# Optimization experiments

Measured on AMD Instinct MI355X. Metric: run time of the kernel, lower is better.

Reference implementation:

```python
import jax, jax.numpy as jnp
import numpy as np

HIDDEN = 4096
N_HEADS = 32
N_KV_HEADS = 8
HEAD_DIM = 128
ROPE_THETA = 1e6
RMS_EPS = 1e-6
SEQ = 2048


def setup_inputs() -> dict:
    key = jax.random.key(0)
    k1, k2, k3 = jax.random.split(key, 3)
    hidden_states = jax.random.normal(k1, (SEQ, HIDDEN), dtype=jnp.float32)
    # fused QKV weight: [hidden, (H + 2*Hkv) * head_dim]
    qkv_out = (N_HEADS + 2 * N_KV_HEADS) * HEAD_DIM
    w_qkv = jax.random.normal(k2, (HIDDEN, qkv_out), dtype=jnp.float32) * (HIDDEN ** -0.5)
    w_o = jax.random.normal(k3, (N_HEADS * HEAD_DIM, HIDDEN), dtype=jnp.float32) * ((N_HEADS * HEAD_DIM) ** -0.5)
    q_norm_w = jnp.ones((HEAD_DIM,), dtype=jnp.float32)
    k_norm_w = jnp.ones((HEAD_DIM,), dtype=jnp.float32)
    # NeoX-style rotary tables [T, head_dim/2]
    pos = jnp.arange(SEQ, dtype=jnp.float32)
    inv_freq = 1.0 / (ROPE_THETA ** (jnp.arange(0, HEAD_DIM, 2, dtype=jnp.float32) / HEAD_DIM))
    freqs = pos[:, None] * inv_freq[None, :]  # [T, d/2]
    cos = jnp.cos(freqs)
    sin = jnp.sin(freqs)
    return {"hidden_states": hidden_states, "cos": cos, "sin": sin,
            "w_qkv": w_qkv, "w_o": w_o, "q_norm_w": q_norm_w, "k_norm_w": k_norm_w}


def _rms_norm(x, w, eps=RMS_EPS):
    # per-head RMSNorm over last dim (head_dim)
    var = jnp.mean(jnp.square(x), axis=-1, keepdims=True)
    return x * jax.lax.rsqrt(var + eps) * w


def _rope(x, cos, sin):
    # NeoX rotate-half: x split into two halves of head_dim
    d2 = x.shape[-1] // 2
    x1, x2 = x[..., :d2], x[..., d2:]
    c = cos[:, None, :]  # [T,1,d/2] broadcast over heads
    s = sin[:, None, :]
    return jnp.concatenate([x1 * c - x2 * s, x2 * c + x1 * s], axis=-1)


def reference(hidden_states, cos, sin, w_qkv, w_o, q_norm_w, k_norm_w):
    T = hidden_states.shape[0]
    H, Hkv, D = N_HEADS, N_KV_HEADS, HEAD_DIM
    G = H // Hkv  # GQA group size
    scale = D ** -0.5

    qkv = hidden_states @ w_qkv  # [T, (H+2Hkv)*D]
    q, k, v = jnp.split(qkv, [H * D, (H + Hkv) * D], axis=1)
    q = q.reshape(T, H, D)
    k = k.reshape(T, Hkv, D)
    v = v.reshape(T, Hkv, D)

    q = _rms_norm(q, q_norm_w)
    k = _rms_norm(k, k_norm_w)
    q = _rope(q, cos, sin)
    k = _rope(k, cos, sin)

    # GQA: group query heads onto shared KV heads
    qg = q.reshape(T, Hkv, G, D)
    scores = jnp.einsum('qhgd,khd->hgqk', qg, k) * scale  # [Hkv,G,T,T]
    causal = jnp.tril(jnp.ones((T, T), dtype=bool))
    scores = jnp.where(causal, scores, jnp.float32(-1e30))
    probs = jax.nn.softmax(scores, axis=-1)
    out = jnp.einsum('hgqk,khd->qhgd', probs, v).reshape(T, H * D)
    return out @ w_o  # [T, hidden]
```

## Files before the change

kernel.cpp:

```cpp
#include <hip/hip_runtime.h>
#include <stdint.h>

#define SEQ   2048
#define HID   4096
#define NQH   32
#define NKVH  8
#define HD    128
#define QKVN  6144

typedef uint16_t u16;
typedef __attribute__((ext_vector_type(8))) short bf16x8;
typedef __attribute__((ext_vector_type(4))) float f32x4;
typedef __attribute__((ext_vector_type(4))) unsigned int u32x4;

static __device__ __forceinline__ float bf2f(u16 h){
  union { float f; unsigned int u; } v; v.u = ((unsigned int)h) << 16; return v.f;
}
static __device__ __forceinline__ u16 f2bf(float f){
  unsigned int u = __float_as_uint(f);
  return (u16)((u + 0x7fffu + ((u >> 16) & 1u)) >> 16);
}
static __device__ __forceinline__ f32x4 mfma16(bf16x8 a, bf16x8 b, f32x4 c){
  return __builtin_amdgcn_mfma_f32_16x16x32_bf16(a, b, c, 0, 0, 0);
}
static __device__ __forceinline__ void gload16(const void* g, void* l){
  __builtin_amdgcn_global_load_lds((const __attribute__((address_space(1))) void*)g,
                                   (__attribute__((address_space(3))) void*)l, 16, 0, 0);
}

__global__ void k_cvt(const float* __restrict__ src, u16* __restrict__ dst, int n4){
  int i = blockIdx.x * blockDim.x + threadIdx.x;
  if (i >= n4) return;
  float4 v = ((const float4*)src)[i];
  uint2 o;
  o.x = (unsigned)f2bf(v.x) | ((unsigned)f2bf(v.y) << 16);
  o.y = (unsigned)f2bf(v.z) | ((unsigned)f2bf(v.w) << 16);
  ((uint2*)dst)[i] = o;
}

__global__ void k_transpose_cvt(const float* __restrict__ src, u16* __restrict__ dst, int K, int N){
  __shared__ float t[32][33];
  int n0 = blockIdx.x * 32, k0 = blockIdx.y * 32;
  int tx = threadIdx.x, ty = threadIdx.y;
#pragma unroll
  for (int i = 0; i < 32; i += 8)
    t[ty + i][tx] = src[(size_t)(k0 + ty + i) * N + n0 + tx];
  __syncthreads();
#pragma unroll
  for (int i = 0; i < 32; i += 8)
    dst[(size_t)(n0 + ty + i) * K + k0 + tx] = f2bf(t[tx][ty + i]);
}

template<int OUTBF>
__global__ __launch_bounds__(256) void k_gemm(const u16* __restrict__ A, const u16* __restrict__ Bt,
                                              void* __restrict__ Cv, int M, int N, int K){
  __shared__ __align__(16) u16 Asm[128][32];
  __shared__ __align__(16) u16 Bsm[128][32];
  int tid = threadIdx.x, lane = tid & 63, wid = tid >> 6;
  int wr = wid >> 1, wc = wid & 1;
  int l16 = lane & 15, lhi = lane >> 4;
  size_t brow = (size_t)blockIdx.y * 128, bcol = (size_t)blockIdx.x * 128;
  const f32x4 vz = {0.f, 0.f, 0.f, 0.f};
  f32x4 acc[4][4];
#pragma unroll
  for (int m = 0; m < 4; m++)
#pragma unroll
    for (int n = 0; n < 4; n++) acc[m][n] = vz;
  int srow = wid * 32 + (lane >> 2);
  int scol = (lane & 3) * 8;
  const u16* Ag = A + (brow + srow) * (size_t)K + scol;
  const u16* Bg = Bt + (bcol + srow) * (size_t)K + scol;
  u16* Al0 = &Asm[wid * 32][0];
  u16* Al1 = &Asm[wid * 32 + 16][0];
  u16* Bl0 = &Bsm[wid * 32][0];
  u16* Bl1 = &Bsm[wid * 32 + 16][0];
  for (int kt = 0; kt < K; kt += 32){
    __syncthreads();
    gload16(Ag + kt, Al0);
    gload16(Ag + (size_t)16 * K + kt, Al1);
    gload16(Bg + kt, Bl0);
    gload16(Bg + (size_t)16 * K + kt, Bl1);
    __syncthreads();
    bf16x8 af[4], bfr[4];
#pragma unroll
    for (int m = 0; m < 4; m++) af[m]  = *(const bf16x8*)&Asm[wr*64 + m*16 + l16][lhi*8];
#pragma unroll
    for (int n = 0; n < 4; n++) bfr[n] = *(const bf16x8*)&Bsm[wc*64 + n*16 + l16][lhi*8];
#pragma unroll
    for (int m = 0; m < 4; m++)
#pragma unroll
      for (int n = 0; n < 4; n++) acc[m][n] = mfma16(af[m], bfr[n], acc[m][n]);
  }
  int rbase = wr*64 + lhi*4, cbase = wc*64 + l16;
#pragma unroll
  for (int m = 0; m < 4; m++)
#pragma unroll
    for (int n = 0; n < 4; n++)
#pragma unroll
      for (int i = 0; i < 4; i++){
        size_t row = brow + rbase + m*16 + i;
        size_t col = bcol + cbase + n*16;
        if (OUTBF) ((u16*)Cv)[row * (size_t)N + col] = f2bf(acc[m][n][i]);
        else       ((float*)Cv)[row * (size_t)N + col] = acc[m][n][i];
      }
}

__global__ __launch_bounds__(256) void k_rmsrope(const u16* __restrict__ qkv, const float* __restrict__ cosp,
                                                 const float* __restrict__ sinp, const float* __restrict__ qw,
                                                 const float* __restrict__ kw, u16* __restrict__ Qr,
                                                 u16* __restrict__ Kr){
  int t = blockIdx.x;
  int lane = threadIdx.x & 63, w = threadIdx.x >> 6;
  int hh = blockIdx.y * 4 + w;
  bool isq = hh < NQH;
  int hl = isq ? hh : hh - NQH;
  const u16* src = qkv + (size_t)t * QKVN + (isq ? hl * HD : NQH * HD + hl * HD);
  unsigned u = *(const unsigned*)(src + 2 * lane);
  float x0 = bf2f((u16)(u & 0xffffu)), x1 = bf2f((u16)(u >> 16));
  float ss = x0 * x0 + x1 * x1;
#pragma unroll
  for (int m = 1; m < 64; m <<= 1) ss += __shfl_xor(ss, m);
  float rs = rsqrtf(ss * (1.f / HD) + 1e-6f);
  const float* wp = isq ? qw : kw;
  float w0 = wp[2 * lane], w1 = wp[2 * lane + 1];
  float xn0 = x0 * rs * w0, xn1 = x1 * rs * w1;
  float p0 = __shfl_xor(xn0, 32), p1 = __shfl_xor(xn1, 32);
  int j0 = (2 * lane) & 63;
  float c0 = cosp[t * 64 + j0], c1 = cosp[t * 64 + j0 + 1];
  float s0 = sinp[t * 64 + j0], s1 = sinp[t * 64 + j0 + 1];
  float o0, o1;
  if (lane < 32){ o0 = xn0 * c0 - p0 * s0; o1 = xn1 * c1 - p1 * s1; }
  else          { o0 = xn0 * c0 + p0 * s0; o1 = xn1 * c1 + p1 * s1; }
  if (isq){ o0 *= 0.08838834764831845f; o1 *= 0.08838834764831845f; }
  u16* dst = isq ? (Qr + ((size_t)hl * SEQ + t) * HD) : (Kr + ((size_t)hl * SEQ + t) * HD);
  *(unsigned*)(dst + 2 * lane) = (unsigned)f2bf(o0) | ((unsigned)f2bf(o1) << 16);
}

__global__ void k_vt(const u16* __restrict__ qkv, u16* __restrict__ VT){
  __shared__ u16 t[32][33];
  int t0 = blockIdx.x * 32, d0 = blockIdx.y * 32, hv = blockIdx.z;
  int tx = threadIdx.x, ty = threadIdx.y;
#pragma unroll
  for (int i = 0; i < 32; i += 8)
    t[ty + i][tx] = qkv[(size_t)(t0 + ty + i) * QKVN + (NQH + NKVH) * HD + hv * HD + d0 + tx];
  __syncthreads();
#pragma unroll
  for (int i = 0; i < 32; i += 8)
    VT[((size_t)hv * HD + d0 + ty + i) * SEQ + t0 + tx] = t[tx][ty + i];
}

__global__ __launch_bounds__(512, 2) void k_attn(const u16* __restrict__ Q, const u16* __restrict__ Kg,
                                                 const u16* __restrict__ VTg, u16* __restrict__ AO){
  __shared__ __align__(16) u16 Ksm[2][64][128];
  __shared__ __align__(16) u16 Vsm[2][128][64];
  __shared__ __align__(16) u16 Psm[8][16][72];
  int tid = threadIdx.x, lane = tid & 63, wid = tid >> 6;
  int l16 = lane & 15, lhi = lane >> 4;
  int bid = blockIdx.x;
  int kvg = bid & 7, rr = bid >> 3;
  int J = 15 - (rr >> 2);
  int hq = kvg * 4 + (rr & 3);
  int qb = J * 128;
  const u16* Kh = Kg  + (size_t)kvg * SEQ * HD;
  const u16* Vh = VTg + (size_t)kvg * HD * SEQ;
  const u16* Qh = Q   + (size_t)hq * SEQ * HD;

  bf16x8 qf[4];
#pragma unroll
  for (int ks = 0; ks < 4; ks++)
    qf[ks] = *(const bf16x8*)(Qh + (size_t)(qb + wid*16 + l16) * HD + ks*32 + lhi*8);

  const f32x4 vz = {0.f, 0.f, 0.f, 0.f};
  f32x4 o[8];
  float mrow[4], lrow[4];
#pragma unroll
  for (int n = 0; n < 8; n++) o[n] = vz;
#pragma unroll
  for (int i = 0; i < 4; i++){ mrow[i] = -1e30f; lrow[i] = 0.f; }

  int krl0 = wid*8 + (lane >> 4), krl1 = krl0 + 4;
  int kgs  = lane & 15;
  const u16* ks0 = Kh + (size_t)krl0 * HD + ((kgs ^ (krl0 & 7)) << 3);
  const u16* ks1 = Kh + (size_t)krl1 * HD + ((kgs ^ (krl1 & 7)) << 3);
  int vrl0 = wid*16 + (lane >> 3), vrl1 = vrl0 + 8;
  int vgs  = lane & 7;
  const u16* vs0 = Vh + (size_t)vrl0 * SEQ + ((vgs ^ (vrl0 & 7)) << 3);
  const u16* vs1 = Vh + (size_t)vrl1 * SEQ + ((vgs ^ (vrl1 & 7)) << 3);

  gload16(ks0, &Ksm[0][wid*8][0]);
  gload16(ks1, &Ksm[0][wid*8 + 4][0]);
  gload16(vs0, &Vsm[0][wid*16][0]);
  gload16(vs1, &Vsm[0][wid*16 + 8][0]);
  __syncthreads();

  int ntr = 2*J + 2;
  int wrow0 = qb + wid*16;
  for (int t = 0; t < ntr; t++){
    int cur = t & 1, nxt = cur ^ 1;
    int kt0 = t << 6;
    if (t < ntr - 1){
      size_t ko = (size_t)(t + 1) * 64 * HD;
      gload16(ks0 + ko, &Ksm[nxt][wid*8][0]);
      gload16(ks1 + ko, &Ksm[nxt][wid*8 + 4][0]);
      int vo = (t + 1) * 64;
      gload16(vs0 + vo, &Vsm[nxt][wid*16][0]);
      gload16(vs1 + vo, &Vsm[nxt][wid*16 + 8][0]);
    }
    if (kt0 <= wrow0 + 15){
      f32x4 s[4];
#pragma unroll
      for (int n = 0; n < 4; n++) s[n] = vz;
      const u16* kbase = &Ksm[cur][0][0];
#pragma unroll
      for (int n = 0; n < 4; n++){
        int row = n*16 + l16, rx = row & 7;
#pragma unroll
        for (int ks = 0; ks < 4; ks++){
          bf16x8 kf = *(const bf16x8*)(kbase + row*128 + (((ks*4 + lhi) ^ rx) << 3));
          s[n] = mfma16(qf[ks], kf, s[n]);
        }
      }
      if (kt0 + 63 > wrow0){
#pragma unroll
        for (int n = 0; n < 4; n++)
#pragma unroll
          for (int i = 0; i < 4; i++)
            if (kt0 + n*16 + l16 > wrow0 + lhi*4 + i) s[n][i] = -1e30f;
      }
#pragma unroll
      for (int i = 0; i < 4; i++){
        float tm = fmaxf(fmaxf(s[0][i], s[1][i]), fmaxf(s[2][i], s[3][i]));
        tm = fmaxf(tm, __shfl_xor(tm, 1));
        tm = fmaxf(tm, __shfl_xor(tm, 2));
        tm = fmaxf(tm, __shfl_xor(tm, 4));
        tm = fmaxf(tm, __shfl_xor(tm, 8));
        float nm = fmaxf(mrow[i], tm);
        float sc = __expf(mrow[i] - nm);
        mrow[i] = nm;
        float rsum = 0.f;
#pragma unroll
        for (int n = 0; n < 4; n++){
          float p = __expf(s[n][i] - nm);
          s[n][i] = p;
          rsum += p;
        }
        rsum += __shfl_xor(rsum, 1);
        rsum += __shfl_xor(rsum, 2);
        rsum += __shfl_xor(rsum, 4);
        rsum += __shfl_xor(rsum, 8);
        lrow[i] = lrow[i] * sc + rsum;
#pragma unroll
        for (int n = 0; n < 8; n++) o[n][i] *= sc;
      }
#pragma unroll
      for (int n = 0; n < 4; n++)
#pragma unroll
        for (int i = 0; i < 4; i++)
          Psm[wid][lhi*4 + i][n*16 + l16] = f2bf(s[n][i]);
      const u16* vbase = &Vsm[cur][0][0];
#pragma unroll
      for (int ksv = 0; ksv < 2; ksv++){
        bf16x8 pa = *(const bf16x8*)&Psm[wid][l16][ksv*32 + lhi*8];
#pragma unroll
        for (int n = 0; n < 8; n++){
          int row = n*16 + l16;
          bf16x8 vb = *(const bf16x8*)(vbase + row*64 + ((((ksv*4) + lhi) ^ (row & 7)) << 3));
          o[n] = mfma16(pa, vb, o[n]);
        }
      }
    }
    if (t < ntr - 1) __syncthreads();
  }
  float inv[4];
#pragma unroll
  for (int i = 0; i < 4; i++) inv[i] = 1.f / lrow[i];
#pragma unroll
  for (int n = 0; n < 8; n++)
#pragma unroll
    for (int i = 0; i < 4; i++){
      int trow = wrow0 + lhi*4 + i;
      AO[(size_t)trow * HID + hq * HD + n*16 + l16] = f2bf(o[n][i] * inv[i]);
    }
}

extern "C" void kernel_launch(void* const* d_in, const int* in_sizes, int n_in,
                              void* d_out, int out_size, void* d_ws, size_t ws_size,
                              hipStream_t stream){
  const float* hs   = (const float*)d_in[0];
  const float* cosp = (const float*)d_in[1];
  const float* sinp = (const float*)d_in[2];
  const float* wqkv = (const float*)d_in[3];
  const float* wo   = (const float*)d_in[4];
  const float* qw   = (const float*)d_in[5];
  const float* kw   = (const float*)d_in[6];
  float* out = (float*)d_out;
  char* ws = (char*)d_ws;
  u16* XB    = (u16*)(ws + 0);
  u16* WQKVT = (u16*)(ws + 16777216);
  u16* WOT   = (u16*)(ws + 0);
  u16* QKV   = (u16*)(ws + 67108864);
  u16* QR    = (u16*)(ws + 92274688);
  u16* KR    = (u16*)(ws + 109051904);
  u16* VTB   = (u16*)(ws + 113246208);
  u16* AOB   = (u16*)(ws + 117440512);

  k_cvt<<<(SEQ * HID / 4 + 255) / 256, 256, 0, stream>>>(hs, XB, SEQ * HID / 4);
  k_transpose_cvt<<<dim3(QKVN / 32, HID / 32), dim3(32, 8), 0, stream>>>(wqkv, WQKVT, HID, QKVN);
  k_gemm<1><<<dim3(QKVN / 128, SEQ / 128), 256, 0, stream>>>(XB, WQKVT, QKV, SEQ, QKVN, HID);
  k_transpose_cvt<<<dim3(HID / 32, HID / 32), dim3(32, 8), 0, stream>>>(wo, WOT, HID, HID);
  k_rmsrope<<<dim3(SEQ, 10), 256, 0, stream>>>(QKV, cosp, sinp, qw, kw, QR, KR);
  k_vt<<<dim3(SEQ / 32, HD / 32, NKVH), dim3(32, 8), 0, stream>>>(QKV, VTB);
  k_attn<<<512, 512, 0, stream>>>(QR, KR, VTB, AOB);
  k_gemm<0><<<dim3(HID / 128, SEQ / 128), 256, 0, stream>>>(AOB, WOT, out, SEQ, HID, HID);
}
```

Measured before the change: 397.6 us.

## Rewrite GEMM with triple-buffered LDS pipeline, 128x256 tiles and swizzled loads

Replaces the GEMM kernel with a 512-thread, 128x256-tile version that triple-buffers K=64 slices in shared memory. Global-to-LDS loads for tile t+2 are interleaved with MFMA phases, coordinated by barriers, explicit waitcnt, sched_barrier and setprio. LDS rows are XOR-swizzled to avoid bank conflicts. The aim is to hide memory latency and remove the serialized load-then-compute pattern of the old single-buffered kernel, at the cost of far more shared memory per block (lower occupancy) and fragile hand-written synchronization.

```diff
diff --git a/kernel.cpp b/kernel.cpp
--- a/kernel.cpp
+++ b/kernel.cpp
@@ -52,56 +52,134 @@
 }
 
 template<int OUTBF>
-__global__ __launch_bounds__(256) void k_gemm(const u16* __restrict__ A, const u16* __restrict__ Bt,
+__global__ __launch_bounds__(512) void k_gemm(const u16* __restrict__ A, const u16* __restrict__ Bt,
                                               void* __restrict__ Cv, int M, int N, int K){
-  __shared__ __align__(16) u16 Asm[128][32];
-  __shared__ __align__(16) u16 Bsm[128][32];
-  int tid = threadIdx.x, lane = tid & 63, wid = tid >> 6;
-  int wr = wid >> 1, wc = wid & 1;
-  int l16 = lane & 15, lhi = lane >> 4;
-  size_t brow = (size_t)blockIdx.y * 128, bcol = (size_t)blockIdx.x * 128;
+  __shared__ __align__(16) u16 Asm[3][128][64];
+  __shared__ __align__(16) u16 Bsm[3][256][64];
+  const int tid = threadIdx.x, lane = tid & 63, wid = tid >> 6;
+  const int wm = wid >> 2, wn = wid & 3;
+  const int l16 = lane & 15, lhi = lane >> 4;
+  const int rx = l16 & 7;
+  const size_t brow = (size_t)blockIdx.y * 128, bcol = (size_t)blockIdx.x * 256;
+
   const f32x4 vz = {0.f, 0.f, 0.f, 0.f};
   f32x4 acc[4][4];
 #pragma unroll
   for (int m = 0; m < 4; m++)
 #pragma unroll
     for (int n = 0; n < 4; n++) acc[m][n] = vz;
-  int srow = wid * 32 + (lane >> 2);
-  int scol = (lane & 3) * 8;
-  const u16* Ag = A + (brow + srow) * (size_t)K + scol;
-  const u16* Bg = Bt + (bcol + srow) * (size_t)K + scol;
-  u16* Al0 = &Asm[wid * 32][0];
-  u16* Al1 = &Asm[wid * 32 + 16][0];
-  u16* Bl0 = &Bsm[wid * 32][0];
-  u16* Bl1 = &Bsm[wid * 32 + 16][0];
-  for (int kt = 0; kt < K; kt += 32){
-    __syncthreads();
-    gload16(Ag + kt, Al0);
-    gload16(Ag + (size_t)16 * K + kt, Al1);
-    gload16(Bg + kt, Bl0);
-    gload16(Bg + (size_t)16 * K + kt, Bl1);
-    __syncthreads();
-    bf16x8 af[4], bfr[4];
-#pragma unroll
-    for (int m = 0; m < 4; m++) af[m]  = *(const bf16x8*)&Asm[wr*64 + m*16 + l16][lhi*8];
-#pragma unroll
-    for (int n = 0; n < 4; n++) bfr[n] = *(const bf16x8*)&Bsm[wc*64 + n*16 + l16][lhi*8];
-#pragma unroll
-    for (int m = 0; m < 4; m++)
-#pragma unroll
-      for (int n = 0; n < 4; n++) acc[m][n] = mfma16(af[m], bfr[n], acc[m][n]);
+
+  const int sg   = (lane & 7) ^ (lane >> 3);
+  const int srow = wid * 8 + (lane >> 3);
+  const u16* Ags = A  + (brow + srow) * (size_t)K + sg * 8;
+  const u16* Bgs = Bt + (bcol + srow) * (size_t)K + sg * 8;
+  const int NT = K >> 6;
+
+#pragma unroll
+  for (int t0 = 0; t0 < 2; t0++){
+    size_t ko = (size_t)t0 * 64;
+    gload16(Ags + ko,                   &Asm[t0][      wid*8][0]);
+    gload16(Ags + (size_t) 64*K + ko,   &Asm[t0][ 64 + wid*8][0]);
+    gload16(Bgs + ko,                   &Bsm[t0][      wid*8][0]);
+    gload16(Bgs + (size_t) 64*K + ko,   &Bsm[t0][ 64 + wid*8][0]);
+    gload16(Bgs + (size_t)128*K + ko,   &Bsm[t0][128 + wid*8][0]);
+    gload16(Bgs + (size_t)192*K + ko,   &Bsm[t0][192 + wid*8][0]);
   }
-  int rbase = wr*64 + lhi*4, cbase = wc*64 + l16;
-#pragma unroll
-  for (int m = 0; m < 4; m++)
-#pragma unroll
-    for (int n = 0; n < 4; n++)
+  asm volatile("s_waitcnt vmcnt(6)" ::: "memory");
+  __builtin_amdgcn_sched_barrier(0);
+  __builtin_amdgcn_s_barrier();
+
+  for (int t = 0; t < NT; ++t){
+    const int c = t % 3, s = (t + 2) % 3;
+    const size_t ko = (size_t)(t + 2) * 64;
+    const bool st = (t + 2 < NT);
+    bf16x8 a0[4], a1[4], b0a, b0b, b1a, b1b;
+#pragma unroll
+    for (int mi = 0; mi < 4; ++mi)
+      a0[mi] = *(const bf16x8*)&Asm[c][wm*64 + mi*16 + l16][(lhi ^ rx) << 3];
+    b0a = *(const bf16x8*)&Bsm[c][wn*64 +  0 + l16][(lhi ^ rx) << 3];
+    b0b = *(const bf16x8*)&Bsm[c][wn*64 + 16 + l16][(lhi ^ rx) << 3];
+    if (st){
+      gload16(Ags + ko,                 &Asm[s][      wid*8][0]);
+      gload16(Ags + (size_t)64*K + ko,  &Asm[s][ 64 + wid*8][0]);
+    }
+    __builtin_amdgcn_s_barrier();
+    asm volatile("s_waitcnt lgkmcnt(0)" ::: "memory");
+    __builtin_amdgcn_sched_barrier(0);
+    __builtin_amdgcn_s_setprio(1);
+#pragma unroll
+    for (int mi = 0; mi < 4; ++mi){
+      acc[mi][0] = mfma16(a0[mi], b0a, acc[mi][0]);
+      acc[mi][1] = mfma16(a0[mi], b0b, acc[mi][1]);
+    }
+    __builtin_amdgcn_s_setprio(0);
+    __builtin_amdgcn_s_barrier();
+    b1a = *(const bf16x8*)&Bsm[c][wn*64 + 32 + l16][(lhi ^ rx) << 3];
+    b1b = *(const bf16x8*)&Bsm[c][wn*64 + 48 + l16][(lhi ^ rx) << 3];
+    if (st) gload16(Bgs + ko, &Bsm[s][wid*8][0]);
+    __builtin_amdgcn_s_barrier();
+    asm volatile("s_waitcnt lgkmcnt(0)" ::: "memory");
+    __builtin_amdgcn_sched_barrier(0);
+    __builtin_amdgcn_s_setprio(1);
+#pragma unroll
+    for (int mi = 0; mi < 4; ++mi){
+      acc[mi][2] = mfma16(a0[mi], b1a, acc[mi][2]);
+      acc[mi][3] = mfma16(a0[mi], b1b, acc[mi][3]);
+    }
+    __builtin_amdgcn_s_setprio(0);
+    __builtin_amdgcn_s_barrier();
+#pragma unroll
+    for (int mi = 0; mi < 4; ++mi)
+      a1[mi] = *(const bf16x8*)&Asm[c][wm*64 + mi*16 + l16][((4 + lhi) ^ rx) << 3];
+    b0a = *(const bf16x8*)&Bsm[c][wn*64 +  0 + l16][((4 + lhi) ^ rx) << 3];
+    b0b = *(const bf16x8*)&Bsm[c][wn*64 + 16 + l16][((4 + lhi) ^ rx) << 3];
+    if (st){
+      gload16(Bgs + (size_t) 64*K + ko, &Bsm[s][ 64 + wid*8][0]);
+      gload16(Bgs + (size_t)128*K + ko, &Bsm[s][128 + wid*8][0]);
+    }
+    __builtin_amdgcn_s_barrier();
+    asm volatile("s_waitcnt lgkmcnt(0)" ::: "memory");
+    __builtin_amdgcn_sched_barrier(0);
+    __builtin_amdgcn_s_setprio(1);
+#pragma unroll
+    for (int mi = 0; mi < 4; ++mi){
+      acc[mi][0] = mfma16(a1[mi], b0a, acc[mi][0]);
+      acc[mi][1] = mfma16(a1[mi], b0b, acc[mi][1]);
+    }
+    __builtin_amdgcn_s_setprio(0);
+    __builtin_amdgcn_s_barrier();
+    b1a = *(const bf16x8*)&Bsm[c][wn*64 + 32 + l16][((4 + lhi) ^ rx) << 3];
+    b1b = *(const bf16x8*)&Bsm[c][wn*64 + 48 + l16][((4 + lhi) ^ rx) << 3];
+    if (st){
+      gload16(Bgs + (size_t)192*K + ko, &Bsm[s][192 + wid*8][0]);
+      asm volatile("s_waitcnt vmcnt(6)" ::: "memory");
+    } else {
+      asm volatile("s_waitcnt vmcnt(0)" ::: "memory");
+    }
+    __builtin_amdgcn_sched_barrier(0);
+    __builtin_amdgcn_s_barrier();
+    asm volatile("s_waitcnt lgkmcnt(0)" ::: "memory");
+    __builtin_amdgcn_sched_barrier(0);
+    __builtin_amdgcn_s_setprio(1);
+#pragma unroll
+    for (int mi = 0; mi < 4; ++mi){
+      acc[mi][2] = mfma16(a1[mi], b1a, acc[mi][2]);
+      acc[mi][3] = mfma16(a1[mi], b1b, acc[mi][3]);
+    }
+    __builtin_amdgcn_s_setprio(0);
+    __builtin_amdgcn_s_barrier();
+  }
+
+#pragma unroll
+  for (int mi = 0; mi < 4; mi++)
+#pragma unroll
+    for (int ni = 0; ni < 4; ni++)
 #pragma unroll
       for (int i = 0; i < 4; i++){
-        size_t row = brow + rbase + m*16 + i;
-        size_t col = bcol + cbase + n*16;
-        if (OUTBF) ((u16*)Cv)[row * (size_t)N + col] = f2bf(acc[m][n][i]);
-        else       ((float*)Cv)[row * (size_t)N + col] = acc[m][n][i];
+        size_t row = brow + wm*64 + mi*16 + lhi*4 + i;
+        size_t col = bcol + wn*64 + ni*16 + l16;
+        if (OUTBF) ((u16*)Cv)[row * (size_t)N + col] = f2bf(acc[mi][ni][i]);
+        else       ((float*)Cv)[row * (size_t)N + col] = acc[mi][ni][i];
       }
 }
 
@@ -213,10 +291,10 @@
       const u16* kbase = &Ksm[cur][0][0];
 #pragma unroll
       for (int n = 0; n < 4; n++){
-        int row = n*16 + l16, rx = row & 7;
+        int row = n*16 + l16, rxk = row & 7;
 #pragma unroll
         for (int ks = 0; ks < 4; ks++){
-          bf16x8 kf = *(const bf16x8*)(kbase + row*128 + (((ks*4 + lhi) ^ rx) << 3));
+          bf16x8 kf = *(const bf16x8*)(kbase + row*128 + (((ks*4 + lhi) ^ rxk) << 3));
           s[n] = mfma16(qf[ks], kf, s[n]);
         }
       }
@@ -306,10 +384,10 @@
 
   k_cvt<<<(SEQ * HID / 4 + 255) / 256, 256, 0, stream>>>(hs, XB, SEQ * HID / 4);
   k_transpose_cvt<<<dim3(QKVN / 32, HID / 32), dim3(32, 8), 0, stream>>>(wqkv, WQKVT, HID, QKVN);
-  k_gemm<1><<<dim3(QKVN / 128, SEQ / 128), 256, 0, stream>>>(XB, WQKVT, QKV, SEQ, QKVN, HID);
+  k_gemm<1><<<dim3(QKVN / 256, SEQ / 128), 512, 0, stream>>>(XB, WQKVT, QKV, SEQ, QKVN, HID);
   k_transpose_cvt<<<dim3(HID / 32, HID / 32), dim3(32, 8), 0, stream>>>(wo, WOT, HID, HID);
   k_rmsrope<<<dim3(SEQ, 10), 256, 0, stream>>>(QKV, cosp, sinp, qw, kw, QR, KR);
   k_vt<<<dim3(SEQ / 32, HD / 32, NKVH), dim3(32, 8), 0, stream>>>(QKV, VTB);
   k_attn<<<512, 512, 0, stream>>>(QR, KR, VTB, AOB);
-  k_gemm<0><<<dim3(HID / 128, SEQ / 128), 256, 0, stream>>>(AOB, WOT, out, SEQ, HID, HID);
-}
+  k_gemm<0><<<dim3(HID / 256, SEQ / 128), 512, 0, stream>>>(AOB, WOT, out, SEQ, HID, HID);
+}
```

New measurement: 459.4 us. 1.16x slower.

## Rewrite GEMM with 4-stage LDS pipeline, 128x256 tiles, swizzle and interleaved MFMA

Applied to the files above, without the earlier changes.

The bf16 GEMM kernel is restructured to use 512 threads and 128x256 output tiles, with a 4-deep ring of LDS buffers filled by direct global-to-LDS loads issued three tiles ahead. Fragment reads for the next tile are interleaved with MFMA groups under explicit waitcnt, sched_barrier and setprio control, and a single s_barrier per k-step replaces the two __syncthreads. An XOR swizzle on the LDS column index is meant to avoid bank conflicts. This aims to hide global and LDS latency in both projections. In exchange it uses more LDS per block, gives fewer blocks for the output GEMM, and depends on fragile hand-tuned wait counts.

```diff
diff --git a/kernel.cpp b/kernel.cpp
--- a/kernel.cpp
+++ b/kernel.cpp
@@ -51,57 +51,114 @@
     dst[(size_t)(n0 + ty + i) * K + k0 + tx] = f2bf(t[tx][ty + i]);
 }
 
+#define FRAG_A(buf, mi) (*(const bf16x8*)&Asm[buf][wm*64 + (mi)*16 + l16][(lhi ^ swz) << 3])
+#define FRAG_B(buf, ni) (*(const bf16x8*)&Bsm[buf][wn*64 + (ni)*16 + l16][(lhi ^ swz) << 3])
+
+#define TILE(T, aC, b01C, b23C, aN, b01N)                                      \
+  do {                                                                         \
+    const int bufc_ = (T) & 3;                                                 \
+    b23C[0] = FRAG_B(bufc_, 2);                                                \
+    b23C[1] = FRAG_B(bufc_, 3);                                                \
+    asm volatile("s_waitcnt lgkmcnt(2)" ::: "memory");                         \
+    __builtin_amdgcn_sched_barrier(0);                                         \
+    __builtin_amdgcn_s_setprio(1);                                             \
+    acc[0][0] = mfma16(aC[0], b01C[0], acc[0][0]);                             \
+    acc[1][0] = mfma16(aC[1], b01C[0], acc[1][0]);                             \
+    acc[2][0] = mfma16(aC[2], b01C[0], acc[2][0]);                             \
+    acc[3][0] = mfma16(aC[3], b01C[0], acc[3][0]);                             \
+    acc[0][1] = mfma16(aC[0], b01C[1], acc[0][1]);                             \
+    acc[1][1] = mfma16(aC[1], b01C[1], acc[1][1]);                             \
+    acc[2][1] = mfma16(aC[2], b01C[1], acc[2][1]);                             \
+    acc[3][1] = mfma16(aC[3], b01C[1], acc[3][1]);                             \
+    __builtin_amdgcn_s_setprio(0);                                             \
+    if ((T) + 1 < NT){                                                         \
+      const int bufn_ = ((T) + 1) & 3;                                         \
+      aN[0] = FRAG_A(bufn_, 0); aN[1] = FRAG_A(bufn_, 1);                      \
+      aN[2] = FRAG_A(bufn_, 2); aN[3] = FRAG_A(bufn_, 3);                      \
+      b01N[0] = FRAG_B(bufn_, 0); b01N[1] = FRAG_B(bufn_, 1);                  \
+      asm volatile("s_waitcnt lgkmcnt(6)" ::: "memory");                       \
+    } else {                                                                   \
+      asm volatile("s_waitcnt lgkmcnt(0)" ::: "memory");                       \
+    }                                                                          \
+    __builtin_amdgcn_sched_barrier(0);                                         \
+    __builtin_amdgcn_s_setprio(1);                                             \
+    acc[0][2] = mfma16(aC[0], b23C[0], acc[0][2]);                             \
+    acc[1][2] = mfma16(aC[1], b23C[0], acc[1][2]);                             \
+    acc[2][2] = mfma16(aC[2], b23C[0], acc[2][2]);                             \
+    acc[3][2] = mfma16(aC[3], b23C[0], acc[3][2]);                             \
+    acc[0][3] = mfma16(aC[0], b23C[1], acc[0][3]);                             \
+    acc[1][3] = mfma16(aC[1], b23C[1], acc[1][3]);                             \
+    acc[2][3] = mfma16(aC[2], b23C[1], acc[2][3]);                             \
+    acc[3][3] = mfma16(aC[3], b23C[1], acc[3][3]);                             \
+    __builtin_amdgcn_s_setprio(0);                                             \
+    if ((T) + 3 < NT){                                                         \
+      const int bufs_ = ((T) + 3) & 3;                                         \
+      const size_t ko_ = (size_t)((T) + 3) * 32;                               \
+      gload16(Ags + ko_, &Asm[bufs_][wid*16][0]);                              \
+      gload16(Bgs + ko_, &Bsm[bufs_][wid*16][0]);                              \
+      gload16(Bgs + (size_t)128*K + ko_, &Bsm[bufs_][128 + wid*16][0]);        \
+      asm volatile("s_waitcnt vmcnt(3)" ::: "memory");                         \
+    } else {                                                                   \
+      asm volatile("s_waitcnt vmcnt(0)" ::: "memory");                         \
+    }                                                                          \
+    __builtin_amdgcn_sched_barrier(0);                                         \
+    __builtin_amdgcn_s_barrier();                                              \
+  } while(0)
+
 template<int OUTBF>
-__global__ __launch_bounds__(256) void k_gemm(const u16* __restrict__ A, const u16* __restrict__ Bt,
+__global__ __launch_bounds__(512) void k_gemm(const u16* __restrict__ A, const u16* __restrict__ Bt,
                                               void* __restrict__ Cv, int M, int N, int K){
-  __shared__ __align__(16) u16 Asm[128][32];
-  __shared__ __align__(16) u16 Bsm[128][32];
-  int tid = threadIdx.x, lane = tid & 63, wid = tid >> 6;
-  int wr = wid >> 1, wc = wid & 1;
-  int l16 = lane & 15, lhi = lane >> 4;
-  size_t brow = (size_t)blockIdx.y * 128, bcol = (size_t)blockIdx.x * 128;
+  __shared__ __align__(16) u16 Asm[4][128][32];
+  __shared__ __align__(16) u16 Bsm[4][256][32];
+  const int tid = threadIdx.x, lane = tid & 63, wid = tid >> 6;
+  const int wm = wid >> 2, wn = wid & 3;
+  const int l16 = lane & 15, lhi = lane >> 4;
+  const int swz = (l16 >> 1) & 3;
+  const size_t brow = (size_t)blockIdx.y * 128, bcol = (size_t)blockIdx.x * 256;
+
   const f32x4 vz = {0.f, 0.f, 0.f, 0.f};
   f32x4 acc[4][4];
 #pragma unroll
   for (int m = 0; m < 4; m++)
 #pragma unroll
     for (int n = 0; n < 4; n++) acc[m][n] = vz;
-  int srow = wid * 32 + (lane >> 2);
-  int scol = (lane & 3) * 8;
-  const u16* Ag = A + (brow + srow) * (size_t)K + scol;
-  const u16* Bg = Bt + (bcol + srow) * (size_t)K + scol;
-  u16* Al0 = &Asm[wid * 32][0];
-  u16* Al1 = &Asm[wid * 32 + 16][0];
-  u16* Bl0 = &Bsm[wid * 32][0];
-  u16* Bl1 = &Bsm[wid * 32 + 16][0];
-  for (int kt = 0; kt < K; kt += 32){
-    __syncthreads();
-    gload16(Ag + kt, Al0);
-    gload16(Ag + (size_t)16 * K + kt, Al1);
-    gload16(Bg + kt, Bl0);
-    gload16(Bg + (size_t)16 * K + kt, Bl1);
-    __syncthreads();
-    bf16x8 af[4], bfr[4];
-#pragma unroll
-    for (int m = 0; m < 4; m++) af[m]  = *(const bf16x8*)&Asm[wr*64 + m*16 + l16][lhi*8];
-#pragma unroll
-    for (int n = 0; n < 4; n++) bfr[n] = *(const bf16x8*)&Bsm[wc*64 + n*16 + l16][lhi*8];
-#pragma unroll
-    for (int m = 0; m < 4; m++)
-#pragma unroll
-      for (int n = 0; n < 4; n++) acc[m][n] = mfma16(af[m], bfr[n], acc[m][n]);
+
+  const int srow = wid * 16 + (lane >> 2);
+  const int sgr  = ((lane & 3) ^ ((lane >> 3) & 3)) * 8;
+  const u16* Ags = A  + (brow + srow) * (size_t)K + sgr;
+  const u16* Bgs = Bt + (bcol + srow) * (size_t)K + sgr;
+  const int NT = K >> 5;
+
+#pragma unroll
+  for (int t0 = 0; t0 < 3; ++t0){
+    const size_t ko = (size_t)t0 * 32;
+    gload16(Ags + ko, &Asm[t0][wid*16][0]);
+    gload16(Bgs + ko, &Bsm[t0][wid*16][0]);
+    gload16(Bgs + (size_t)128*K + ko, &Bsm[t0][128 + wid*16][0]);
   }
-  int rbase = wr*64 + lhi*4, cbase = wc*64 + l16;
-#pragma unroll
-  for (int m = 0; m < 4; m++)
-#pragma unroll
-    for (int n = 0; n < 4; n++)
+  asm volatile("s_waitcnt vmcnt(3)" ::: "memory");
+  __builtin_amdgcn_sched_barrier(0);
+  __builtin_amdgcn_s_barrier();
+
+  bf16x8 aA[4], aB[4], b01A[2], b01B[2], b23A[2], b23B[2];
+  aA[0] = FRAG_A(0, 0); aA[1] = FRAG_A(0, 1); aA[2] = FRAG_A(0, 2); aA[3] = FRAG_A(0, 3);
+  b01A[0] = FRAG_B(0, 0); b01A[1] = FRAG_B(0, 1);
+
+  for (int u = 0; u < (NT >> 1); ++u){
+    TILE(2*u,     aA, b01A, b23A, aB, b01B);
+    TILE(2*u + 1, aB, b01B, b23B, aA, b01A);
+  }
+
+#pragma unroll
+  for (int mi = 0; mi < 4; mi++)
+#pragma unroll
+    for (int ni = 0; ni < 4; ni++)
 #pragma unroll
       for (int i = 0; i < 4; i++){
-        size_t row = brow + rbase + m*16 + i;
-        size_t col = bcol + cbase + n*16;
-        if (OUTBF) ((u16*)Cv)[row * (size_t)N + col] = f2bf(acc[m][n][i]);
-        else       ((float*)Cv)[row * (size_t)N + col] = acc[m][n][i];
+        size_t row = brow + wm*64 + mi*16 + lhi*4 + i;
+        size_t col = bcol + wn*64 + ni*16 + l16;
+        if (OUTBF) ((u16*)Cv)[row * (size_t)N + col] = f2bf(acc[mi][ni][i]);
+        else       ((float*)Cv)[row * (size_t)N + col] = acc[mi][ni][i];
       }
 }
 
@@ -213,10 +270,10 @@
       const u16* kbase = &Ksm[cur][0][0];
 #pragma unroll
       for (int n = 0; n < 4; n++){
-        int row = n*16 + l16, rx = row & 7;
+        int row = n*16 + l16, rxk = row & 7;
 #pragma unroll
         for (int ks = 0; ks < 4; ks++){
-          bf16x8 kf = *(const bf16x8*)(kbase + row*128 + (((ks*4 + lhi) ^ rx) << 3));
+          bf16x8 kf = *(const bf16x8*)(kbase + row*128 + (((ks*4 + lhi) ^ rxk) << 3));
           s[n] = mfma16(qf[ks], kf, s[n]);
         }
       }
@@ -306,10 +363,10 @@
 
   k_cvt<<<(SEQ * HID / 4 + 255) / 256, 256, 0, stream>>>(hs, XB, SEQ * HID / 4);
   k_transpose_cvt<<<dim3(QKVN / 32, HID / 32), dim3(32, 8), 0, stream>>>(wqkv, WQKVT, HID, QKVN);
-  k_gemm<1><<<dim3(QKVN / 128, SEQ / 128), 256, 0, stream>>>(XB, WQKVT, QKV, SEQ, QKVN, HID);
+  k_gemm<1><<<dim3(QKVN / 256, SEQ / 128), 512, 0, stream>>>(XB, WQKVT, QKV, SEQ, QKVN, HID);
   k_transpose_cvt<<<dim3(HID / 32, HID / 32), dim3(32, 8), 0, stream>>>(wo, WOT, HID, HID);
   k_rmsrope<<<dim3(SEQ, 10), 256, 0, stream>>>(QKV, cosp, sinp, qw, kw, QR, KR);
   k_vt<<<dim3(SEQ / 32, HD / 32, NKVH), dim3(32, 8), 0, stream>>>(QKV, VTB);
   k_attn<<<512, 512, 0, stream>>>(QR, KR, VTB, AOB);
-  k_gemm<0><<<dim3(HID / 128, SEQ / 128), 256, 0, stream>>>(AOB, WOT, out, SEQ, HID, HID);
-}
+  k_gemm<0><<<dim3(HID / 256, SEQ / 128), 512, 0, stream>>>(AOB, WOT, out, SEQ, HID, HID);
+}
```

After: 411.4 us. 1.03x slower.

## Rewrite GEMM with larger tiles, 4-stage LDS pipeline and swizzled loads

Applied to the files above, without the earlier changes.

Replaces the single-buffered 128x128 GEMM with a templated 512-thread kernel that uses 256x256 or 128x256 tiles. A 4-slot shared-memory ring is filled three stages ahead, with explicit vmcnt/lgkmcnt waits, double-buffered register fragments and raised priority around the MFMA block. An XOR swizzle on the LDS column is meant to cut bank conflicts. The goal is to hide global load latency and raise MFMA utilisation for the QKV and output projections, at the cost of more LDS and registers per block, which may lower occupancy.

```diff
diff --git a/kernel.cpp b/kernel.cpp
--- a/kernel.cpp
+++ b/kernel.cpp
@@ -51,57 +51,103 @@
     dst[(size_t)(n0 + ty + i) * K + k0 + tx] = f2bf(t[tx][ty + i]);
 }
 
-template<int OUTBF>
-__global__ __launch_bounds__(256) void k_gemm(const u16* __restrict__ A, const u16* __restrict__ Bt,
+template<int MI, int OUTBF>
+__global__ __launch_bounds__(512) void k_gemm(const u16* __restrict__ A, const u16* __restrict__ Bt,
                                               void* __restrict__ Cv, int M, int N, int K){
-  __shared__ __align__(16) u16 Asm[128][32];
-  __shared__ __align__(16) u16 Bsm[128][32];
-  int tid = threadIdx.x, lane = tid & 63, wid = tid >> 6;
-  int wr = wid >> 1, wc = wid & 1;
-  int l16 = lane & 15, lhi = lane >> 4;
-  size_t brow = (size_t)blockIdx.y * 128, bcol = (size_t)blockIdx.x * 128;
+  constexpr int BM  = MI * 32;
+  constexpr int LPB = (MI == 8) ? 4 : 3;
+  constexpr int RPB = MI + 4;
+  __shared__ __align__(16) u16 Asm[4][BM][32];
+  __shared__ __align__(16) u16 Bsm[4][256][32];
+  const int tid = threadIdx.x, lane = tid & 63, wid = tid >> 6;
+  const int wm = wid >> 2, wn = wid & 3;
+  const int l16 = lane & 15, lhi = lane >> 4;
+  const int swz = (l16 >> 1) & 3;
+  const size_t brow = (size_t)blockIdx.y * BM, bcol = (size_t)blockIdx.x * 256;
+
   const f32x4 vz = {0.f, 0.f, 0.f, 0.f};
-  f32x4 acc[4][4];
-#pragma unroll
-  for (int m = 0; m < 4; m++)
+  f32x4 acc[MI][4];
+#pragma unroll
+  for (int m = 0; m < MI; m++)
 #pragma unroll
     for (int n = 0; n < 4; n++) acc[m][n] = vz;
-  int srow = wid * 32 + (lane >> 2);
-  int scol = (lane & 3) * 8;
-  const u16* Ag = A + (brow + srow) * (size_t)K + scol;
-  const u16* Bg = Bt + (bcol + srow) * (size_t)K + scol;
-  u16* Al0 = &Asm[wid * 32][0];
-  u16* Al1 = &Asm[wid * 32 + 16][0];
-  u16* Bl0 = &Bsm[wid * 32][0];
-  u16* Bl1 = &Bsm[wid * 32 + 16][0];
-  for (int kt = 0; kt < K; kt += 32){
-    __syncthreads();
-    gload16(Ag + kt, Al0);
-    gload16(Ag + (size_t)16 * K + kt, Al1);
-    gload16(Bg + kt, Bl0);
-    gload16(Bg + (size_t)16 * K + kt, Bl1);
-    __syncthreads();
-    bf16x8 af[4], bfr[4];
-#pragma unroll
-    for (int m = 0; m < 4; m++) af[m]  = *(const bf16x8*)&Asm[wr*64 + m*16 + l16][lhi*8];
-#pragma unroll
-    for (int n = 0; n < 4; n++) bfr[n] = *(const bf16x8*)&Bsm[wc*64 + n*16 + l16][lhi*8];
-#pragma unroll
-    for (int m = 0; m < 4; m++)
-#pragma unroll
-      for (int n = 0; n < 4; n++) acc[m][n] = mfma16(af[m], bfr[n], acc[m][n]);
+
+  const int rsub = lane >> 2;
+  const int gsrc = ((lane & 3) ^ ((lane >> 3) & 3)) * 8;
+  const u16* Ag = A  + (brow + (MI == 8 ? wid * 32 : wid * 16) + rsub) * (size_t)K + gsrc;
+  const u16* Bg = Bt + (bcol + wid * 32 + rsub) * (size_t)K + gsrc;
+  const int NH = K >> 5;
+
+#define STAGE(H) do{                                                            \
+    const int sl_ = (H) & 3; const size_t ko_ = (size_t)(H) * 32;               \
+    if (MI == 8){                                                               \
+      gload16(Ag + ko_,                  &Asm[sl_][wid*32][0]);                 \
+      gload16(Ag + (size_t)16*K + ko_,   &Asm[sl_][wid*32 + 16][0]);            \
+    } else {                                                                    \
+      gload16(Ag + ko_,                  &Asm[sl_][wid*16][0]);                 \
+    }                                                                           \
+    gload16(Bg + ko_,                    &Bsm[sl_][wid*32][0]);                 \
+    gload16(Bg + (size_t)16*K + ko_,     &Bsm[sl_][wid*32 + 16][0]);            \
+  }while(0)
+
+#define RDFRAGS(H, aS, bS) do{                                                  \
+    const int sl_ = (H) & 3;                                                    \
+    _Pragma("unroll")                                                           \
+    for (int mi = 0; mi < MI; mi++)                                             \
+      aS[mi] = *(const bf16x8*)&Asm[sl_][wm*(BM/2) + mi*16 + l16][(lhi ^ swz) << 3]; \
+    _Pragma("unroll")                                                           \
+    for (int ni = 0; ni < 4; ni++)                                              \
+      bS[ni] = *(const bf16x8*)&Bsm[sl_][wn*64 + ni*16 + l16][(lhi ^ swz) << 3]; \
+  }while(0)
+
+#define BODY(H, aC, bC, aN, bN) do{                                             \
+    __builtin_amdgcn_s_barrier();                                               \
+    if ((H) + 3 < NH){                                                          \
+      STAGE((H) + 3);                                                           \
+      asm volatile("s_waitcnt vmcnt(%0)" :: "i"(LPB) : "memory");               \
+    } else {                                                                    \
+      asm volatile("s_waitcnt vmcnt(0)" ::: "memory");                          \
+    }                                                                           \
+    if ((H) + 1 < NH){                                                          \
+      RDFRAGS((H) + 1, aN, bN);                                                 \
+      asm volatile("s_waitcnt lgkmcnt(%0)" :: "i"(RPB) : "memory");             \
+    } else {                                                                    \
+      asm volatile("s_waitcnt lgkmcnt(0)" ::: "memory");                        \
+    }                                                                           \
+    __builtin_amdgcn_sched_barrier(0);                                          \
+    __builtin_amdgcn_s_setprio(1);                                              \
+    _Pragma("unroll")                                                           \
+    for (int mi = 0; mi < MI; mi++)                                             \
+      _Pragma("unroll")                                                         \
+      for (int ni = 0; ni < 4; ni++)                                            \
+        acc[mi][ni] = mfma16(aC[mi], bC[ni], acc[mi][ni]);                      \
+    __builtin_amdgcn_s_setprio(0);                                              \
+  }while(0)
+
+  STAGE(0); STAGE(1); STAGE(2);
+  asm volatile("s_waitcnt vmcnt(0)" ::: "memory");
+  __builtin_amdgcn_s_barrier();
+  bf16x8 aX[MI], bX[4], aY[MI], bY[4];
+  RDFRAGS(0, aX, bX);
+
+  for (int u = 0; u < (NH >> 1); ++u){
+    BODY(2*u,     aX, bX, aY, bY);
+    BODY(2*u + 1, aY, bY, aX, bX);
   }
-  int rbase = wr*64 + lhi*4, cbase = wc*64 + l16;
-#pragma unroll
-  for (int m = 0; m < 4; m++)
-#pragma unroll
-    for (int n = 0; n < 4; n++)
+#undef STAGE
+#undef RDFRAGS
+#undef BODY
+
+#pragma unroll
+  for (int mi = 0; mi < MI; mi++)
+#pragma unroll
+    for (int ni = 0; ni < 4; ni++)
 #pragma unroll
       for (int i = 0; i < 4; i++){
-        size_t row = brow + rbase + m*16 + i;
-        size_t col = bcol + cbase + n*16;
-        if (OUTBF) ((u16*)Cv)[row * (size_t)N + col] = f2bf(acc[m][n][i]);
-        else       ((float*)Cv)[row * (size_t)N + col] = acc[m][n][i];
+        size_t row = brow + wm*(BM/2) + mi*16 + lhi*4 + i;
+        size_t col = bcol + wn*64 + ni*16 + l16;
+        if (OUTBF) ((u16*)Cv)[row * (size_t)N + col] = f2bf(acc[mi][ni][i]);
+        else       ((float*)Cv)[row * (size_t)N + col] = acc[mi][ni][i];
       }
 }
 
@@ -213,10 +259,10 @@
       const u16* kbase = &Ksm[cur][0][0];
 #pragma unroll
       for (int n = 0; n < 4; n++){
-        int row = n*16 + l16, rx = row & 7;
+        int row = n*16 + l16, rxk = row & 7;
 #pragma unroll
         for (int ks = 0; ks < 4; ks++){
-          bf16x8 kf = *(const bf16x8*)(kbase + row*128 + (((ks*4 + lhi) ^ rx) << 3));
+          bf16x8 kf = *(const bf16x8*)(kbase + row*128 + (((ks*4 + lhi) ^ rxk) << 3));
           s[n] = mfma16(qf[ks], kf, s[n]);
         }
       }
@@ -306,10 +352,10 @@
 
   k_cvt<<<(SEQ * HID / 4 + 255) / 256, 256, 0, stream>>>(hs, XB, SEQ * HID / 4);
   k_transpose_cvt<<<dim3(QKVN / 32, HID / 32), dim3(32, 8), 0, stream>>>(wqkv, WQKVT, HID, QKVN);
-  k_gemm<1><<<dim3(QKVN / 128, SEQ / 128), 256, 0, stream>>>(XB, WQKVT, QKV, SEQ, QKVN, HID);
+  k_gemm<8, 1><<<dim3(QKVN / 256, SEQ / 256), 512, 0, stream>>>(XB, WQKVT, QKV, SEQ, QKVN, HID);
   k_transpose_cvt<<<dim3(HID / 32, HID / 32), dim3(32, 8), 0, stream>>>(wo, WOT, HID, HID);
   k_rmsrope<<<dim3(SEQ, 10), 256, 0, stream>>>(QKV, cosp, sinp, qw, kw, QR, KR);
   k_vt<<<dim3(SEQ / 32, HD / 32, NKVH), dim3(32, 8), 0, stream>>>(QKV, VTB);
   k_attn<<<512, 512, 0, stream>>>(QR, KR, VTB, AOB);
-  k_gemm<0><<<dim3(HID / 128, SEQ / 128), 256, 0, stream>>>(AOB, WOT, out, SEQ, HID, HID);
-}
+  k_gemm<4, 0><<<dim3(HID / 256, SEQ / 128), 512, 0, stream>>>(AOB, WOT, out, SEQ, HID, HID);
+}
```

Result: slower. 423.7 us (+6.6%).
